# Performance work log

Measured on AMD Instinct MI355X. Metric: run time of the kernel, lower is better.

The kernel has to match this reference:

```python
import jax, jax.numpy as jnp
from jax import lax
import numpy as np

B, N, NPOINT, NSAMPLE, RADIUS = 8, 16384, 1024, 32, 0.4
C_IN = 64


def fps(xyz, npoint):
    """Furthest point sampling. xyz: (B, N, 3) -> (B, npoint) int32 indices.
    Matches the CUDA kernel: start from index 0, iteratively pick argmax of
    the running min-distance to the selected set."""
    Bb, Nn, _ = xyz.shape

    def step(carry, _):
        min_d, last = carry
        p = jnp.take_along_axis(xyz, last[:, None, None], axis=1)  # (B,1,3)
        d = jnp.sum((xyz - p) ** 2, axis=-1)                       # (B,N)
        min_d = jnp.minimum(min_d, d)
        nxt = jnp.argmax(min_d, axis=1).astype(jnp.int32)
        return (min_d, nxt), nxt

    idx0 = jnp.zeros((Bb,), jnp.int32)
    min_d0 = jnp.full((Bb, Nn), jnp.inf, xyz.dtype)
    _, rest = lax.scan(step, (min_d0, idx0), None, length=npoint - 1)  # (npoint-1, B)
    return jnp.transpose(jnp.concatenate([idx0[None, :], rest], axis=0))  # (B, npoint)


def ball_query(xyz, new_xyz, radius, nsample):
    """xyz: (B,N,3), new_xyz: (B,P,3) -> (B,P,nsample) int32 indices.
    First nsample in-radius indices (ascending), short balls padded with the
    first found index (the centroid itself is always in-radius)."""
    Nn = xyz.shape[1]
    d2 = jnp.sum((new_xyz[:, :, None, :] - xyz[:, None, :, :]) ** 2, axis=-1)  # (B,P,N)
    ar = jnp.arange(Nn, dtype=jnp.int32)
    key = jnp.where(d2 <= radius * radius, ar, Nn)  # out-of-ball -> sentinel N
    neg_top, _ = lax.top_k(-key, nsample)           # nsample smallest keys
    gidx = -neg_top                                  # (B,P,nsample)
    return jnp.where(gidx == Nn, gidx[..., :1], gidx)


def setup_inputs() -> dict:
    key = jax.random.key(0)
    ks = jax.random.split(key, 8)
    return {
        "xyz": jax.random.normal(ks[0], (B, N, 3), jnp.float32),
        "features": jax.random.normal(ks[1], (B, C_IN, N), jnp.float32),
        "W1": jax.random.normal(ks[2], (64, 3 + C_IN), jnp.float32) * 0.05,
        "b1": jax.random.normal(ks[3], (64,), jnp.float32) * 0.05,
        "W2": jax.random.normal(ks[4], (64, 64), jnp.float32) * 0.05,
        "b2": jax.random.normal(ks[5], (64,), jnp.float32) * 0.05,
        "W3": jax.random.normal(ks[6], (128, 64), jnp.float32) * 0.05,
        "b3": jax.random.normal(ks[7], (128,), jnp.float32) * 0.05,
    }


def reference(xyz, features, W1, b1, W2, b2, W3, b3):
    Bb = xyz.shape[0]
    idx = fps(xyz, NPOINT)                                         # (B,P)
    new_xyz = jnp.take_along_axis(xyz, idx[:, :, None], axis=1)    # (B,P,3)

    gidx = ball_query(xyz, new_xyz, RADIUS, NSAMPLE)               # (B,P,S)
    bi = jnp.arange(Bb)[:, None, None]
    grouped_xyz = xyz[bi, gidx] - new_xyz[:, :, None, :]           # (B,P,S,3) relative coords
    feats_t = jnp.transpose(features, (0, 2, 1))                   # (B,N,C)
    grouped_feats = feats_t[bi, gidx]                              # (B,P,S,C)
    h = jnp.concatenate([grouped_xyz, grouped_feats], axis=-1)     # (B,P,S,3+C)

    # shared per-point MLP (1x1 convs) + ReLU
    h = jax.nn.relu(jnp.einsum('bpsc,oc->bpso', h, W1) + b1)
    h = jax.nn.relu(jnp.einsum('bpsc,oc->bpso', h, W2) + b2)
    h = jax.nn.relu(jnp.einsum('bpsc,oc->bpso', h, W3) + b3)

    pooled = jnp.max(h, axis=2)                                    # (B,P,128) max over nsample
    new_features = jnp.transpose(pooled, (0, 2, 1))                # (B,128,P)
    return new_xyz, new_features
```

## Files before the change

### kernel.cpp

```cpp
#include <hip/hip_runtime.h>

#define R2 0.16f

typedef float f32x2 __attribute__((ext_vector_type(2)));

__device__ __forceinline__ float sqd(float x, float y, float z,
                                     float px, float py, float pz) {
  float dx = __fsub_rn(x, px);
  float dy = __fsub_rn(y, py);
  float dz = __fsub_rn(z, pz);
  return __fadd_rn(__fadd_rn(__fmul_rn(dx, dx), __fmul_rn(dy, dy)),
                   __fmul_rn(dz, dz));
}

__device__ __forceinline__ float wave64_max_dpp(float x) {
#define DPP_STEP(CTRL)                                                      \
  {                                                                         \
    int t_ = __builtin_amdgcn_update_dpp(__float_as_int(x),                 \
                                         __float_as_int(x), CTRL, 0xf, 0xf, \
                                         false);                            \
    x = fmaxf(x, __int_as_float(t_));                                       \
  }
  DPP_STEP(0x111) DPP_STEP(0x112) DPP_STEP(0x114)
  DPP_STEP(0x118) DPP_STEP(0x142) DPP_STEP(0x143)
#undef DPP_STEP
  return x;
}
__device__ __forceinline__ unsigned wave64_min_dpp_u32(unsigned x) {
#define DPP_STEP(CTRL)                                                      \
  {                                                                         \
    unsigned t_ = (unsigned)__builtin_amdgcn_update_dpp(                    \
        (int)x, (int)x, CTRL, 0xf, 0xf, false);                             \
    x = (t_ < x) ? t_ : x;                                                  \
  }
  DPP_STEP(0x111) DPP_STEP(0x112) DPP_STEP(0x114)
  DPP_STEP(0x118) DPP_STEP(0x142) DPP_STEP(0x143)
#undef DPP_STEP
  return x;
}

__global__ __launch_bounds__(256) void zero_hist(unsigned* __restrict__ h) {
  h[blockIdx.x * 256 + threadIdx.x] = 0u;
}

__global__ __launch_bounds__(256) void hist_kernel(const float* __restrict__ xyz,
                                                   unsigned* __restrict__ hist,
                                                   unsigned* __restrict__ rank,
                                                   unsigned* __restrict__ cid) {
  int t = blockIdx.x * 256 + threadIdx.x;
  int b = t >> 14;
  const float* p = xyz + (size_t)t * 3;
  int cx = (int)floorf(p[0] + 4.0f);
  int cy = (int)floorf(p[1] + 4.0f);
  int cz = (int)floorf(p[2] + 4.0f);
  cx = min(max(cx, 0), 7);
  cy = min(max(cy, 0), 7);
  cz = min(max(cz, 0), 7);
  unsigned c = (unsigned)(cx | (cy << 3) | (cz << 6));
  unsigned r = atomicAdd(&hist[(b << 9) + c], 1u);
  rank[t] = r;
  cid[t] = c;
}

__global__ __launch_bounds__(512) void scan_kernel(const unsigned* __restrict__ hist,
                                                   unsigned* __restrict__ starts) {
  __shared__ unsigned a[512];
  int b = blockIdx.x, t = threadIdx.x;
  unsigned h = hist[(b << 9) + t];
  a[t] = h;
  __syncthreads();
  for (int s = 1; s < 512; s <<= 1) {
    unsigned v = (t >= s) ? a[t - s] : 0u;
    __syncthreads();
    a[t] += v;
    __syncthreads();
  }
  starts[(b << 9) + t] = a[t] - h;
}

__global__ __launch_bounds__(256) void scatter_kernel(
    const float* __restrict__ xyz, const unsigned* __restrict__ starts,
    const unsigned* __restrict__ rank, const unsigned* __restrict__ cid,
    float* __restrict__ xs2, float* __restrict__ ys2, float* __restrict__ zs2,
    unsigned* __restrict__ oi2) {
  int t = blockIdx.x * 256 + threadIdx.x;
  int b = t >> 14, n = t & 16383;
  unsigned pos = starts[(b << 9) + cid[t]] + rank[t];
  const float* p = xyz + (size_t)t * 3;
  size_t o = ((size_t)b << 14) + pos;
  xs2[o] = p[0];
  ys2[o] = p[1];
  zs2[o] = p[2];
  oi2[o] = (unsigned)n;
}

__global__ __launch_bounds__(1024) void fps_kernel(
    const float* __restrict__ xyz, const float* __restrict__ xs,
    const float* __restrict__ ys, const float* __restrict__ zs,
    const unsigned* __restrict__ oi, int* __restrict__ idx_out) {
#pragma clang fp contract(off)
  extern __shared__ float4 xylds[];
  __shared__ unsigned long long s_gkey[3];
  __shared__ float s_cd[3][3][16];
  int b = blockIdx.x;
  int tid = threadIdx.x;
  int lane = tid & 63, wid = tid >> 6;
  const float* xb = xyz + (size_t)b * 16384 * 3;
  int base = tid << 4;
  const float4* xv = (const float4*)(xs + ((size_t)b << 14) + base);
  const float4* yv = (const float4*)(ys + ((size_t)b << 14) + base);
  const float4* zv = (const float4*)(zs + ((size_t)b << 14) + base);
  const uint4* ov = (const uint4*)(oi + ((size_t)b << 14) + base);
  float xr[16], yr[16], zr[16];
  unsigned OI[16];
#pragma unroll
  for (int q = 0; q < 4; ++q) {
    *(float4*)(xr + 4 * q) = xv[q];
    *(float4*)(yr + 4 * q) = yv[q];
    *(float4*)(zr + 4 * q) = zv[q];
    *(uint4*)(OI + 4 * q) = ov[q];
  }
  float bxl = xr[0], bxh = xr[0], byl = yr[0], byh = yr[0], bzl = zr[0],
        bzh = zr[0];
#pragma unroll
  for (int k = 1; k < 16; ++k) {
    bxl = fminf(bxl, xr[k]); bxh = fmaxf(bxh, xr[k]);
    byl = fminf(byl, yr[k]); byh = fmaxf(byh, yr[k]);
    bzl = fminf(bzl, zr[k]); bzh = fmaxf(bzh, zr[k]);
  }
  f32x2 Z[8], M[8];
#pragma unroll
  for (int q = 0; q < 8; ++q) {
    xylds[(q << 10) + tid] =
        make_float4(xr[2 * q], xr[2 * q + 1], yr[2 * q], yr[2 * q + 1]);
    Z[q] = {zr[2 * q], zr[2 * q + 1]};
    M[q] = {__builtin_inff(), __builtin_inff()};
  }
  if (tid == 0) idx_out[b * 1024] = 0;
  if (tid < 3) s_gkey[tid] = 0ull;
  __syncthreads();
  float px = xb[0], py = xb[1], pz = xb[2];
  float tv = __builtin_inff();
  for (int it = 1; it < 1024; ++it) {
    int sl = it % 3;
    int slp2 = (sl + 2) % 3;
    float ddx = fmaxf(fmaxf(bxl - px, px - bxh), 0.0f);
    float ddy = fmaxf(fmaxf(byl - py, py - byh), 0.0f);
    float ddz = fmaxf(fmaxf(bzl - pz, pz - bzh), 0.0f);
    float lb = (ddx * ddx + ddy * ddy + ddz * ddz) * 0.999f;
    if (lb < tv) {
      f32x2 px2 = {px, px}, py2 = {py, py}, pz2 = {pz, pz};
      float ntv = -1.0f;
#pragma unroll
      for (int q = 0; q < 8; ++q) {
        float4 t = xylds[(q << 10) + tid];
        f32x2 X = {t.x, t.y};
        f32x2 Y = {t.z, t.w};
        f32x2 dx = X - px2;
        f32x2 dy = Y - py2;
        f32x2 dz = Z[q] - pz2;
        f32x2 d = dx * dx + dy * dy + dz * dz;
        M[q].x = fminf(M[q].x, d.x);
        M[q].y = fminf(M[q].y, d.y);
        ntv = fmaxf(fmaxf(ntv, M[q].x), M[q].y);
      }
      tv = ntv;
    }
    float bv = wave64_max_dpp(tv);
    unsigned bvb = (unsigned)__builtin_amdgcn_readlane(__float_as_int(bv), 63);
    float bvf = __int_as_float((int)bvb);
    unsigned long long gk0 = __hip_atomic_load(
        &s_gkey[sl], __ATOMIC_RELAXED, __HIP_MEMORY_SCOPE_WORKGROUP);
    if (bvb >= (unsigned)(gk0 >> 18)) {
      unsigned coi = 0xffffffffu;
      float wx = 0.0f, wy = 0.0f, wz = 0.0f;
      if (tv == bvf) {
#pragma unroll
        for (int q = 0; q < 8; ++q) {
          float4 t = xylds[(q << 10) + tid];
          if (M[q].x == bvf && OI[2 * q] < coi) {
            coi = OI[2 * q]; wx = t.x; wy = t.z; wz = Z[q].x;
          }
          if (M[q].y == bvf && OI[2 * q + 1] < coi) {
            coi = OI[2 * q + 1]; wx = t.y; wy = t.w; wz = Z[q].y;
          }
        }
      }
      unsigned woi = wave64_min_dpp_u32(coi);
      if (coi == woi && coi != 0xffffffffu) {
        s_cd[sl][0][wid] = wx;
        s_cd[sl][1][wid] = wy;
        s_cd[sl][2][wid] = wz;
        unsigned long long key = ((unsigned long long)bvb << 18) |
                                 ((unsigned long long)(16383u - woi) << 4) |
                                 (unsigned long long)wid;
        atomicMax(&s_gkey[sl], key);
      }
    }
    __syncthreads();
    unsigned long long gk = s_gkey[sl];
    if (tid == 0) s_gkey[slp2] = 0ull;
    int w2 = (int)(gk & 15ull);
    int j = 16383 - (int)((gk >> 4) & 0x3fffull);
    px = s_cd[sl][0][w2];
    py = s_cd[sl][1][w2];
    pz = s_cd[sl][2][w2];
    if (tid == 0) idx_out[b * 1024 + it] = j;
  }
}

__global__ __launch_bounds__(256) void gather_newxyz(const float* __restrict__ xyz,
                                                     const int* __restrict__ idx,
                                                     float* __restrict__ out) {
  int t = blockIdx.x * 256 + threadIdx.x;
  int b = t >> 10;
  int i = idx[t];
  const float* src = xyz + ((size_t)b * 16384 + i) * 3;
  float* dst = out + (size_t)t * 3;
  dst[0] = src[0];
  dst[1] = src[1];
  dst[2] = src[2];
}

__global__ __launch_bounds__(256) void transpose_feats(const float* __restrict__ f,
                                                       float* __restrict__ fT) {
  __shared__ float tile[64][65];
  int b = blockIdx.x >> 8;
  int n0 = (blockIdx.x & 255) << 6;
  int t = threadIdx.x;
  int nn = t & 63, c0 = t >> 6;
#pragma unroll
  for (int r = 0; r < 64; r += 4) {
    int c = c0 + r;
    tile[c][nn] = f[((size_t)b * 64 + c) * 16384 + n0 + nn];
  }
  __syncthreads();
  int cc = t & 63, n1 = t >> 6;
#pragma unroll
  for (int r = 0; r < 64; r += 4) {
    int n = n1 + r;
    fT[((size_t)b * 16384 + n0 + n) * 64 + cc] = tile[cc][n];
  }
}

__global__ __launch_bounds__(256) void ballquery_grid(
    const float* __restrict__ xs, const float* __restrict__ ys,
    const float* __restrict__ zs, const unsigned* __restrict__ oi,
    const unsigned* __restrict__ hist, const unsigned* __restrict__ starts,
    const float* __restrict__ newxyz, int* __restrict__ gidx) {
  __shared__ unsigned bm[4][512];
  __shared__ unsigned sfirst[4];
  int wid = threadIdx.x >> 6, lane = threadIdx.x & 63;
  int cid = blockIdx.x * 4 + wid;
  int b = cid >> 10;
  float cx = newxyz[cid * 3 + 0];
  float cy = newxyz[cid * 3 + 1];
  float cz = newxyz[cid * 3 + 2];
  unsigned* mybm = bm[wid];
#pragma unroll
  for (int k = 0; k < 8; ++k) mybm[(k << 6) + lane] = 0u;
  int clox = min(max((int)floorf(cx - 0.4f + 4.0f), 0), 7);
  int chix = min(max((int)floorf(cx + 0.4f + 4.0f), 0), 7);
  int cloy = min(max((int)floorf(cy - 0.4f + 4.0f), 0), 7);
  int chiy = min(max((int)floorf(cy + 0.4f + 4.0f), 0), 7);
  int cloz = min(max((int)floorf(cz - 0.4f + 4.0f), 0), 7);
  int chiz = min(max((int)floorf(cz + 0.4f + 4.0f), 0), 7);
  const float* xsb = xs + ((size_t)b << 14);
  const float* ysb = ys + ((size_t)b << 14);
  const float* zsb = zs + ((size_t)b << 14);
  const unsigned* oib = oi + ((size_t)b << 14);
  const unsigned* hb = hist + (b << 9);
  const unsigned* sb = starts + (b << 9);
  for (int zz = cloz; zz <= chiz; ++zz)
    for (int yy = cloy; yy <= chiy; ++yy)
      for (int xx = clox; xx <= chix; ++xx) {
        unsigned cc = (unsigned)(xx | (yy << 3) | (zz << 6));
        unsigned st = sb[cc], cnt = hb[cc];
        for (unsigned c0 = 0; c0 < cnt; c0 += 64) {
          unsigned g = c0 + (unsigned)lane;
          if (g < cnt) {
            unsigned p = st + g;
            float d2 = sqd(xsb[p], ysb[p], zsb[p], cx, cy, cz);
            if (d2 <= R2) {
              unsigned o = oib[p];
              atomicOr(&mybm[o >> 5], 1u << (o & 31));
            }
          }
        }
      }
  int* out = gidx + (size_t)cid * 32;
  unsigned running = 0;
  for (int s = 0; s < 4 && running < 32; ++s) {
    unsigned lo = mybm[(s << 7) + 2 * lane];
    unsigned hi = mybm[(s << 7) + 2 * lane + 1];
    unsigned long long W = ((unsigned long long)hi << 32) | lo;
    int c = __popcll(W);
    int incl = c;
#pragma unroll
    for (int d = 1; d < 64; d <<= 1) {
      int t = __shfl_up(incl, d);
      if (lane >= d) incl += t;
    }
    int total = __shfl(incl, 63);
    int basep = (int)running + incl - c;
    while (W != 0ull && basep < 32) {
      int t = (int)__builtin_ctzll(W);
      W &= W - 1ull;
      int idxv = (((s << 6) + lane) << 6) + t;
      if (basep == 0) sfirst[wid] = (unsigned)idxv;
      out[basep] = idxv;
      ++basep;
    }
    running += (unsigned)total;
  }
  unsigned nf = running < 32u ? running : 32u;
  unsigned first = sfirst[wid];
  for (unsigned s2 = nf + (unsigned)lane; s2 < 32u; s2 += 64u)
    out[s2] = (int)first;
}

#define FMA16(BASEPTR)                                                     \
  do {                                                                     \
    const float4* hp_ = (const float4*)(BASEPTR);                          \
    float4 v0 = hp_[0], v1 = hp_[1], v2 = hp_[2], v3 = hp_[3];             \
    float a = acc[s];                                                      \
    a = fmaf(w[0], v0.x, a);  a = fmaf(w[1], v0.y, a);                     \
    a = fmaf(w[2], v0.z, a);  a = fmaf(w[3], v0.w, a);                     \
    a = fmaf(w[4], v1.x, a);  a = fmaf(w[5], v1.y, a);                     \
    a = fmaf(w[6], v1.z, a);  a = fmaf(w[7], v1.w, a);                     \
    a = fmaf(w[8], v2.x, a);  a = fmaf(w[9], v2.y, a);                     \
    a = fmaf(w[10], v2.z, a); a = fmaf(w[11], v2.w, a);                    \
    a = fmaf(w[12], v3.x, a); a = fmaf(w[13], v3.y, a);                    \
    a = fmaf(w[14], v3.z, a); a = fmaf(w[15], v3.w, a);                    \
    acc[s] = a;                                                            \
  } while (0)

__global__ __launch_bounds__(256) void mlp_kernel(
    const float* __restrict__ xyz, const float* __restrict__ feats,
    const float* __restrict__ featsT, const float* __restrict__ newxyz,
    const int* __restrict__ gidx,
    const float* __restrict__ W1, const float* __restrict__ b1,
    const float* __restrict__ W2, const float* __restrict__ b2,
    const float* __restrict__ W3, const float* __restrict__ b3,
    float* __restrict__ out, int useT) {
  __shared__ float buf[4][32 * 68];
  int wid = threadIdx.x >> 6, lane = threadIdx.x & 63;
  int cid = blockIdx.x * 4 + wid;
  int b = cid >> 10, p = cid & 1023;
  float* A = buf[wid];
  const int* gi = gidx + (size_t)cid * 32;
  float cx = newxyz[cid * 3 + 0];
  float cy = newxyz[cid * 3 + 1];
  float cz = newxyz[cid * 3 + 2];

  if (useT) {
    const float4* fT4 = (const float4*)(featsT + (size_t)b * 16384 * 64);
    for (int t = lane; t < 512; t += 64) {
      int s = t >> 4, q = t & 15;
      int g = gi[s];
      float4 v = fT4[(size_t)g * 16 + q];
      *(float4*)(A + s * 68 + q * 4) = v;
    }
  } else {
    const float* fb = feats + (size_t)b * 64 * 16384;
    for (int t = lane; t < 2048; t += 64) {
      int c = t >> 5, s = t & 31;
      int g = gi[s];
      A[s * 68 + c] = fb[(size_t)c * 16384 + g];
    }
  }
  for (int t = lane; t < 96; t += 64) {
    int s = t / 3, c = t - s * 3;
    int g = gi[s];
    float pv = xyz[((size_t)b * 16384 + g) * 3 + c];
    float cv = (c == 0) ? cx : ((c == 1) ? cy : cz);
    A[s * 68 + 64 + c] = __fsub_rn(pv, cv);
  }
  if (lane < 32) A[lane * 68 + 67] = 0.0f;
  __syncthreads();

  int o = lane;
  float acc[32];

#pragma unroll
  for (int s = 0; s < 32; ++s) acc[s] = b1[o];
  {
    const float* wr = W1 + o * 67;
    for (int cb = 0; cb < 4; ++cb) {
      float w[16];
#pragma unroll
      for (int q = 0; q < 16; ++q) w[q] = wr[3 + cb * 16 + q];
#pragma unroll
      for (int s = 0; s < 32; ++s) { FMA16(A + s * 68 + cb * 16); }
    }
    float w0 = wr[0], w1 = wr[1], w2 = wr[2];
#pragma unroll
    for (int s = 0; s < 32; ++s) {
      float a = acc[s];
      a = fmaf(w0, A[s * 68 + 64], a);
      a = fmaf(w1, A[s * 68 + 65], a);
      a = fmaf(w2, A[s * 68 + 66], a);
      acc[s] = a;
    }
  }
  __syncthreads();
#pragma unroll
  for (int s = 0; s < 32; ++s) A[s * 64 + o] = fmaxf(acc[s], 0.0f);
  __syncthreads();

#pragma unroll
  for (int s = 0; s < 32; ++s) acc[s] = b2[o];
  {
    const float* wr = W2 + o * 64;
    for (int cb = 0; cb < 4; ++cb) {
      float w[16];
#pragma unroll
      for (int q = 0; q < 16; ++q) w[q] = wr[cb * 16 + q];
#pragma unroll
      for (int s = 0; s < 32; ++s) { FMA16(A + s * 64 + cb * 16); }
    }
  }
  __syncthreads();
#pragma unroll
  for (int s = 0; s < 32; ++s) A[s * 64 + o] = fmaxf(acc[s], 0.0f);
  __syncthreads();

  float* outp = out + 24576;
  for (int po = 0; po < 2; ++po) {
    int o2 = lane + (po << 6);
#pragma unroll
    for (int s = 0; s < 32; ++s) acc[s] = b3[o2];
    const float* wr = W3 + o2 * 64;
    for (int cb = 0; cb < 4; ++cb) {
      float w[16];
#pragma unroll
      for (int q = 0; q < 16; ++q) w[q] = wr[cb * 16 + q];
#pragma unroll
      for (int s = 0; s < 32; ++s) { FMA16(A + s * 64 + cb * 16); }
    }
    float mx = 0.0f;
#pragma unroll
    for (int s = 0; s < 32; ++s) mx = fmaxf(mx, acc[s]);
    outp[((size_t)b * 128 + o2) * 1024 + p] = mx;
  }
}

extern "C" void kernel_launch(void* const* d_in, const int* in_sizes, int n_in,
                              void* d_out, int out_size, void* d_ws, size_t ws_size,
                              hipStream_t stream) {
  const float* xyz = (const float*)d_in[0];
  const float* feats = (const float*)d_in[1];
  const float* W1 = (const float*)d_in[2];
  const float* b1 = (const float*)d_in[3];
  const float* W2 = (const float*)d_in[4];
  const float* b2 = (const float*)d_in[5];
  const float* W3 = (const float*)d_in[6];
  const float* b3 = (const float*)d_in[7];
  float* out = (float*)d_out;

  char* w = (char*)d_ws;
  int* idx = (int*)w;
  int* gidx = (int*)(w + 32768);
  unsigned* hist = (unsigned*)(w + 1081344);
  unsigned* starts = (unsigned*)(w + 1097728);
  unsigned* rank = (unsigned*)(w + 1114112);
  unsigned* cid = (unsigned*)(w + 1638400);
  unsigned* oi2 = (unsigned*)(w + 2162688);
  float* xs2 = (float*)(w + 2686976);
  float* ys2 = (float*)(w + 3211264);
  float* zs2 = (float*)(w + 3735552);
  float* featsT = (float*)(w + 4259840);
  size_t needT = 4259840 + (size_t)8 * 16384 * 64 * sizeof(float);
  int useT = (ws_size >= needT) ? 1 : 0;

  zero_hist<<<16, 256, 0, stream>>>(hist);
  hist_kernel<<<512, 256, 0, stream>>>(xyz, hist, rank, cid);
  scan_kernel<<<8, 512, 0, stream>>>(hist, starts);
  scatter_kernel<<<512, 256, 0, stream>>>(xyz, starts, rank, cid, xs2, ys2,
                                          zs2, oi2);
  fps_kernel<<<8, 1024, 131072, stream>>>(xyz, xs2, ys2, zs2, oi2, idx);
  gather_newxyz<<<32, 256, 0, stream>>>(xyz, idx, out);
  if (useT) transpose_feats<<<2048, 256, 0, stream>>>(feats, featsT);
  ballquery_grid<<<2048, 256, 0, stream>>>(xs2, ys2, zs2, oi2, hist, starts,
                                           out, gidx);
  mlp_kernel<<<2048, 256, 0, stream>>>(xyz, feats, featsT, out, gidx,
                                       W1, b1, W2, b2, W3, b3, out, useT);
}
```

Baseline: 1.999 ms.

## Fuse feature transpose and new_xyz gather into FPS kernel, add wave-level culling

The FPS kernel gains 512 extra blocks that transpose the features in their spare grid space, so that work overlaps with the 8 serial FPS blocks and the separate launch goes away. The new_xyz gather moves into FPS itself, written by thread 0 each iteration. A wave-level bounding box lower bound is added so a whole wave can skip the distance update and the DPP max reduction when no point in it can beat the wave's current max. The cost is a larger launch that uses 128KB of LDS per block, which may limit how the transpose blocks co-schedule, plus extra per-iteration branching.

```diff
diff --git a/kernel.cpp b/kernel.cpp
--- a/kernel.cpp
+++ b/kernel.cpp
@@ -20,6 +20,19 @@
                                          __float_as_int(x), CTRL, 0xf, 0xf, \
                                          false);                            \
     x = fmaxf(x, __int_as_float(t_));                                       \
+  }
+  DPP_STEP(0x111) DPP_STEP(0x112) DPP_STEP(0x114)
+  DPP_STEP(0x118) DPP_STEP(0x142) DPP_STEP(0x143)
+#undef DPP_STEP
+  return x;
+}
+__device__ __forceinline__ float wave64_min_dpp_f32(float x) {
+#define DPP_STEP(CTRL)                                                      \
+  {                                                                         \
+    int t_ = __builtin_amdgcn_update_dpp(__float_as_int(x),                 \
+                                         __float_as_int(x), CTRL, 0xf, 0xf, \
+                                         false);                            \
+    x = fminf(x, __int_as_float(t_));                                       \
   }
   DPP_STEP(0x111) DPP_STEP(0x112) DPP_STEP(0x114)
   DPP_STEP(0x118) DPP_STEP(0x142) DPP_STEP(0x143)
@@ -97,13 +110,36 @@
 __global__ __launch_bounds__(1024) void fps_kernel(
     const float* __restrict__ xyz, const float* __restrict__ xs,
     const float* __restrict__ ys, const float* __restrict__ zs,
-    const unsigned* __restrict__ oi, int* __restrict__ idx_out) {
+    const unsigned* __restrict__ oi, int* __restrict__ idx_out,
+    float* __restrict__ newxyz_out, const float* __restrict__ feats,
+    float* __restrict__ featsT) {
 #pragma clang fp contract(off)
   extern __shared__ float4 xylds[];
   __shared__ unsigned long long s_gkey[3];
   __shared__ float s_cd[3][3][16];
+  int tid = threadIdx.x;
+  if (blockIdx.x >= 8) {
+    int sub = tid >> 8, t = tid & 255;
+    int tileid = (blockIdx.x - 8) * 4 + sub;
+    int b = tileid >> 8;
+    int n0 = (tileid & 255) << 6;
+    float* tile = ((float*)xylds) + sub * 4160;
+    int nn = t & 63, c0 = t >> 6;
+#pragma unroll
+    for (int r = 0; r < 64; r += 4) {
+      int c = c0 + r;
+      tile[c * 65 + nn] = feats[((size_t)b * 64 + c) * 16384 + n0 + nn];
+    }
+    __syncthreads();
+    int cc = t & 63, n1 = t >> 6;
+#pragma unroll
+    for (int r = 0; r < 64; r += 4) {
+      int n = n1 + r;
+      featsT[((size_t)b * 16384 + n0 + n) * 64 + cc] = tile[cc * 65 + n];
+    }
+    return;
+  }
   int b = blockIdx.x;
-  int tid = threadIdx.x;
   int lane = tid & 63, wid = tid >> 6;
   const float* xb = xyz + (size_t)b * 16384 * 3;
   int base = tid << 4;
@@ -128,6 +164,18 @@
     byl = fminf(byl, yr[k]); byh = fmaxf(byh, yr[k]);
     bzl = fminf(bzl, zr[k]); bzh = fmaxf(bzh, zr[k]);
   }
+  float wbxl = __int_as_float(
+      __builtin_amdgcn_readlane(__float_as_int(wave64_min_dpp_f32(bxl)), 63));
+  float wbxh = __int_as_float(
+      __builtin_amdgcn_readlane(__float_as_int(wave64_max_dpp(bxh)), 63));
+  float wbyl = __int_as_float(
+      __builtin_amdgcn_readlane(__float_as_int(wave64_min_dpp_f32(byl)), 63));
+  float wbyh = __int_as_float(
+      __builtin_amdgcn_readlane(__float_as_int(wave64_max_dpp(byh)), 63));
+  float wbzl = __int_as_float(
+      __builtin_amdgcn_readlane(__float_as_int(wave64_min_dpp_f32(bzl)), 63));
+  float wbzh = __int_as_float(
+      __builtin_amdgcn_readlane(__float_as_int(wave64_max_dpp(bzh)), 63));
   f32x2 Z[8], M[8];
 #pragma unroll
   for (int q = 0; q < 8; ++q) {
@@ -136,39 +184,50 @@
     Z[q] = {zr[2 * q], zr[2 * q + 1]};
     M[q] = {__builtin_inff(), __builtin_inff()};
   }
-  if (tid == 0) idx_out[b * 1024] = 0;
+  if (tid == 0) {
+    idx_out[b * 1024] = 0;
+    float* o0 = newxyz_out + (size_t)b * 1024 * 3;
+    o0[0] = xb[0]; o0[1] = xb[1]; o0[2] = xb[2];
+  }
   if (tid < 3) s_gkey[tid] = 0ull;
   __syncthreads();
   float px = xb[0], py = xb[1], pz = xb[2];
   float tv = __builtin_inff();
+  float bvf = __builtin_inff();
+  unsigned bvb = 0x7f800000u;
+  int sl = 1, slp2 = 0;
   for (int it = 1; it < 1024; ++it) {
-    int sl = it % 3;
-    int slp2 = (sl + 2) % 3;
-    float ddx = fmaxf(fmaxf(bxl - px, px - bxh), 0.0f);
-    float ddy = fmaxf(fmaxf(byl - py, py - byh), 0.0f);
-    float ddz = fmaxf(fmaxf(bzl - pz, pz - bzh), 0.0f);
-    float lb = (ddx * ddx + ddy * ddy + ddz * ddz) * 0.999f;
-    if (lb < tv) {
-      f32x2 px2 = {px, px}, py2 = {py, py}, pz2 = {pz, pz};
-      float ntv = -1.0f;
-#pragma unroll
-      for (int q = 0; q < 8; ++q) {
-        float4 t = xylds[(q << 10) + tid];
-        f32x2 X = {t.x, t.y};
-        f32x2 Y = {t.z, t.w};
-        f32x2 dx = X - px2;
-        f32x2 dy = Y - py2;
-        f32x2 dz = Z[q] - pz2;
-        f32x2 d = dx * dx + dy * dy + dz * dz;
-        M[q].x = fminf(M[q].x, d.x);
-        M[q].y = fminf(M[q].y, d.y);
-        ntv = fmaxf(fmaxf(ntv, M[q].x), M[q].y);
+    float wdx = fmaxf(fmaxf(wbxl - px, px - wbxh), 0.0f);
+    float wdy = fmaxf(fmaxf(wbyl - py, py - wbyh), 0.0f);
+    float wdz = fmaxf(fmaxf(wbzl - pz, pz - wbzh), 0.0f);
+    float wlb = (wdx * wdx + wdy * wdy + wdz * wdz) * 0.999f;
+    if (wlb < bvf) {
+      float ddx = fmaxf(fmaxf(bxl - px, px - bxh), 0.0f);
+      float ddy = fmaxf(fmaxf(byl - py, py - byh), 0.0f);
+      float ddz = fmaxf(fmaxf(bzl - pz, pz - bzh), 0.0f);
+      float lb = (ddx * ddx + ddy * ddy + ddz * ddz) * 0.999f;
+      if (lb < tv) {
+        f32x2 px2 = {px, px}, py2 = {py, py}, pz2 = {pz, pz};
+        float ntv = -1.0f;
+#pragma unroll
+        for (int q = 0; q < 8; ++q) {
+          float4 t = xylds[(q << 10) + tid];
+          f32x2 X = {t.x, t.y};
+          f32x2 Y = {t.z, t.w};
+          f32x2 dx = X - px2;
+          f32x2 dy = Y - py2;
+          f32x2 dz = Z[q] - pz2;
+          f32x2 d = dx * dx + dy * dy + dz * dz;
+          M[q].x = fminf(M[q].x, d.x);
+          M[q].y = fminf(M[q].y, d.y);
+          ntv = fmaxf(fmaxf(ntv, M[q].x), M[q].y);
+        }
+        tv = ntv;
       }
-      tv = ntv;
-    }
-    float bv = wave64_max_dpp(tv);
-    unsigned bvb = (unsigned)__builtin_amdgcn_readlane(__float_as_int(bv), 63);
-    float bvf = __int_as_float((int)bvb);
+      float bv = wave64_max_dpp(tv);
+      bvb = (unsigned)__builtin_amdgcn_readlane(__float_as_int(bv), 63);
+      bvf = __int_as_float((int)bvb);
+    }
     unsigned long long gk0 = __hip_atomic_load(
         &s_gkey[sl], __ATOMIC_RELAXED, __HIP_MEMORY_SCOPE_WORKGROUP);
     if (bvb >= (unsigned)(gk0 >> 18)) {
@@ -205,41 +264,13 @@
     px = s_cd[sl][0][w2];
     py = s_cd[sl][1][w2];
     pz = s_cd[sl][2][w2];
-    if (tid == 0) idx_out[b * 1024 + it] = j;
-  }
-}
-
-__global__ __launch_bounds__(256) void gather_newxyz(const float* __restrict__ xyz,
-                                                     const int* __restrict__ idx,
-                                                     float* __restrict__ out) {
-  int t = blockIdx.x * 256 + threadIdx.x;
-  int b = t >> 10;
-  int i = idx[t];
-  const float* src = xyz + ((size_t)b * 16384 + i) * 3;
-  float* dst = out + (size_t)t * 3;
-  dst[0] = src[0];
-  dst[1] = src[1];
-  dst[2] = src[2];
-}
-
-__global__ __launch_bounds__(256) void transpose_feats(const float* __restrict__ f,
-                                                       float* __restrict__ fT) {
-  __shared__ float tile[64][65];
-  int b = blockIdx.x >> 8;
-  int n0 = (blockIdx.x & 255) << 6;
-  int t = threadIdx.x;
-  int nn = t & 63, c0 = t >> 6;
-#pragma unroll
-  for (int r = 0; r < 64; r += 4) {
-    int c = c0 + r;
-    tile[c][nn] = f[((size_t)b * 64 + c) * 16384 + n0 + nn];
-  }
-  __syncthreads();
-  int cc = t & 63, n1 = t >> 6;
-#pragma unroll
-  for (int r = 0; r < 64; r += 4) {
-    int n = n1 + r;
-    fT[((size_t)b * 16384 + n0 + n) * 64 + cc] = tile[cc][n];
+    if (tid == 0) {
+      idx_out[b * 1024 + it] = j;
+      float* o = newxyz_out + ((size_t)b * 1024 + it) * 3;
+      o[0] = px; o[1] = py; o[2] = pz;
+    }
+    sl = (sl == 2) ? 0 : sl + 1;
+    slp2 = (slp2 == 2) ? 0 : slp2 + 1;
   }
 }
 
@@ -478,9 +509,8 @@
   scan_kernel<<<8, 512, 0, stream>>>(hist, starts);
   scatter_kernel<<<512, 256, 0, stream>>>(xyz, starts, rank, cid, xs2, ys2,
                                           zs2, oi2);
-  fps_kernel<<<8, 1024, 131072, stream>>>(xyz, xs2, ys2, zs2, oi2, idx);
-  gather_newxyz<<<32, 256, 0, stream>>>(xyz, idx, out);
-  if (useT) transpose_feats<<<2048, 256, 0, stream>>>(feats, featsT);
+  fps_kernel<<<useT ? 520 : 8, 1024, 131072, stream>>>(
+      xyz, xs2, ys2, zs2, oi2, idx, out, feats, featsT);
   ballquery_grid<<<2048, 256, 0, stream>>>(xs2, ys2, zs2, oi2, hist, starts,
                                            out, gidx);
   mlp_kernel<<<2048, 256, 0, stream>>>(xyz, feats, featsT, out, gidx,
```

Result: faster. 1.935 ms (median of 2 runs) (-3.2%).
